# Kernel optimization log

Measured on AMD Instinct MI355X. Metric: run time of the kernel, lower is better.

## Reference

```python
import jax, jax.numpy as jnp
import numpy as np

B, H, S, D = 2, 16, 2048, 64
DEGREE = 2
EPS = 1e-4


def setup_inputs() -> dict:
    key = jax.random.key(0)
    kq, kk, kv = jax.random.split(key, 3)
    q = jax.random.normal(kq, (B, H, S, D), dtype=jnp.float32)
    k = jax.random.normal(kk, (B, H, S, D), dtype=jnp.float32)
    v = jax.random.normal(kv, (B, H, S, D), dtype=jnp.float32)
    return {"q": q, "k": k, "v": v}


def reference(q, k, v):
    # dots: [B,H,S,S] = QK^T
    dots = jnp.einsum("bhsd,bhtd->bhst", q, k)
    # polynomial kernel: x^degree, row-normalized with clamped denom
    x = dots ** DEGREE
    denom = jnp.maximum(x.sum(axis=-1, keepdims=True), EPS)
    attn = x / denom
    # weighted V sum: [B,H,S,D]
    return jnp.einsum("bhst,bhtd->bhsd", attn, v)
```

## Files before the change

kernel.cpp:

```cpp
#include <hip/hip_runtime.h>


#define S_LEN 2048
#define DH    64
#define BQ    128
#define BK    64
#define LSTR  72
#define PSTR  65
#define BH_N  32
#define PER_BH (S_LEN * DH)
#define NT    (S_LEN / BK)

typedef __bf16 bf16x8 __attribute__((ext_vector_type(8)));
typedef __bf16 bf16x2 __attribute__((ext_vector_type(2)));
typedef float  f32x4  __attribute__((ext_vector_type(4)));

__device__ __forceinline__ unsigned short f2bf(float f) {
    union { float f; unsigned int u; } x; x.f = f;
    unsigned int u = x.u;
    return (unsigned short)((u + 0x7fffu + ((u >> 16) & 1u)) >> 16);
}

__device__ __forceinline__ unsigned int pack2bf(float lo, float hi) {
#if __has_builtin(__builtin_amdgcn_cvt_pk_bf16_f32)
    bf16x2 p = __builtin_amdgcn_cvt_pk_bf16_f32(lo, hi);
    union { bf16x2 v; unsigned int u; } c; c.v = p;
    return c.u;
#else
    return (unsigned int)f2bf(lo) | ((unsigned int)f2bf(hi) << 16);
#endif
}

__global__ __launch_bounds__(256)
void prepass_kernel(const float* __restrict__ kg, const float* __restrict__ vg,
                    unsigned short* __restrict__ kbf, unsigned short* __restrict__ vt)
{
    __shared__ unsigned short Ls[64 * PSTR];
    const int tid = threadIdx.x;
    const int bh  = blockIdx.y;
    const int t0  = blockIdx.x * 64;
    const size_t base = (size_t)bh * PER_BH + (size_t)t0 * DH;

    {
        const float4* src = (const float4*)(kg + base + (size_t)tid * 16);
        float4 a = src[0], b = src[1], c = src[2], d = src[3];
        union { unsigned short h[8]; uint4 v; } u0, u1;
        u0.h[0]=f2bf(a.x); u0.h[1]=f2bf(a.y); u0.h[2]=f2bf(a.z); u0.h[3]=f2bf(a.w);
        u0.h[4]=f2bf(b.x); u0.h[5]=f2bf(b.y); u0.h[6]=f2bf(b.z); u0.h[7]=f2bf(b.w);
        u1.h[0]=f2bf(c.x); u1.h[1]=f2bf(c.y); u1.h[2]=f2bf(c.z); u1.h[3]=f2bf(c.w);
        u1.h[4]=f2bf(d.x); u1.h[5]=f2bf(d.y); u1.h[6]=f2bf(d.z); u1.h[7]=f2bf(d.w);
        uint4* dst = (uint4*)(kbf + base + (size_t)tid * 16);
        dst[0] = u0.v; dst[1] = u1.v;
    }

    const float* vb = vg + base;
    #pragma unroll
    for (int r = 0; r < 4; ++r) {
        int idx = r * 256 + tid;
        int row = idx >> 4, c4 = idx & 15;
        float4 f = ((const float4*)vb)[idx];
        unsigned short* p = &Ls[row * PSTR + c4 * 4];
        p[0] = f2bf(f.x); p[1] = f2bf(f.y); p[2] = f2bf(f.z); p[3] = f2bf(f.w);
    }
    __syncthreads();
    #pragma unroll
    for (int r = 0; r < 2; ++r) {
        int idx = r * 256 + tid;
        int d = idx >> 3, j8 = idx & 7;
        union { unsigned short h[8]; uint4 v; } u;
        #pragma unroll
        for (int jj = 0; jj < 8; ++jj) u.h[jj] = Ls[(j8 * 8 + jj) * PSTR + d];
        *(uint4*)(vt + (size_t)bh * PER_BH + (size_t)d * S_LEN + t0 + j8 * 8) = u.v;
    }
}

__global__ __launch_bounds__(256, 2)
void poly_attn_main(const float* __restrict__ qg,
                    const unsigned short* __restrict__ kbf,
                    const unsigned short* __restrict__ vtbf,
                    float* __restrict__ og)
{
    __shared__ unsigned short Ks[2][BK * LSTR];
    __shared__ unsigned short Vts[2][DH * LSTR];
    __shared__ unsigned short Xs[BQ * LSTR];

    const int tid  = threadIdx.x;
    const int lane = tid & 63;
    const int w    = tid >> 6;
    const int c    = lane & 15;
    const int quad = lane >> 4;

    const int bh = blockIdx.y;
    const int q0 = blockIdx.x * BQ;

    const float* qb = qg + ((size_t)bh * S_LEN + q0) * DH;
    const unsigned short* kb  = kbf  + (size_t)bh * PER_BH;
    const unsigned short* vtb = vtbf + (size_t)bh * PER_BH;
    float* ob = og + ((size_t)bh * S_LEN + q0) * DH;

    bf16x8 qfrag[2][2];
    #pragma unroll
    for (int s = 0; s < 2; ++s) {
        #pragma unroll
        for (int kh = 0; kh < 2; ++kh) {
            const float* qp = qb + (32 * w + 16 * s + c) * DH + kh * 32 + quad * 8;
            float4 f0 = *(const float4*)qp;
            float4 f1 = *(const float4*)(qp + 4);
            union { unsigned int d[4]; bf16x8 v; } u;
            u.d[0] = pack2bf(f0.x, f0.y);
            u.d[1] = pack2bf(f0.z, f0.w);
            u.d[2] = pack2bf(f1.x, f1.y);
            u.d[3] = pack2bf(f1.z, f1.w);
            qfrag[s][kh] = u.v;
        }
    }

    f32x4 oacc[2][4];
    #pragma unroll
    for (int s = 0; s < 2; ++s)
        #pragma unroll
        for (int t = 0; t < 4; ++t) {
            oacc[s][t][0]=0.f; oacc[s][t][1]=0.f; oacc[s][t][2]=0.f; oacc[s][t][3]=0.f;
        }
    float dsum[2] = {0.f, 0.f};

    const int srow = tid >> 3;
    const int sc8  = tid & 7;

    uint4 kreg[2], vreg[2];
    #pragma unroll
    for (int it = 0; it < 2; ++it) {
        int row = srow + it * 32;
        kreg[it] = *(const uint4*)(kb + (size_t)row * DH + sc8 * 8);
        vreg[it] = *(const uint4*)(vtb + (size_t)row * S_LEN + sc8 * 8);
    }
    #pragma unroll
    for (int it = 0; it < 2; ++it) {
        int row = srow + it * 32;
        *(uint4*)&Ks[0][row * LSTR + sc8 * 8] = kreg[it];
        *(uint4*)&Vts[0][row * LSTR + sc8 * 8] = vreg[it];
    }
    __syncthreads();

    for (int t = 0; t < NT; ++t) {
        const int cur = t & 1;
        if (t + 1 < NT) {
            const int t0n = (t + 1) * BK;
            #pragma unroll
            for (int it = 0; it < 2; ++it) {
                int row = srow + it * 32;
                kreg[it] = *(const uint4*)(kb + (size_t)(t0n + row) * DH + sc8 * 8);
                vreg[it] = *(const uint4*)(vtb + (size_t)row * S_LEN + t0n + sc8 * 8);
            }
        }

        f32x4 xaccT[2][4];
        #pragma unroll
        for (int s = 0; s < 2; ++s)
            #pragma unroll
            for (int jt = 0; jt < 4; ++jt) {
                xaccT[s][jt][0]=0.f; xaccT[s][jt][1]=0.f; xaccT[s][jt][2]=0.f; xaccT[s][jt][3]=0.f;
            }
        #pragma unroll
        for (int kh = 0; kh < 2; ++kh) {
            #pragma unroll
            for (int jt = 0; jt < 4; ++jt) {
                bf16x8 kfrag = *(const bf16x8*)&Ks[cur][(jt * 16 + c) * LSTR + kh * 32 + quad * 8];
                #pragma unroll
                for (int s = 0; s < 2; ++s)
                    xaccT[s][jt] = __builtin_amdgcn_mfma_f32_16x16x32_bf16(kfrag, qfrag[s][kh], xaccT[s][jt], 0, 0, 0);
            }
        }

        #pragma unroll
        for (int s = 0; s < 2; ++s) {
            #pragma unroll
            for (int jt = 0; jt < 4; ++jt) {
                float x0 = xaccT[s][jt][0], x1 = xaccT[s][jt][1];
                float x2 = xaccT[s][jt][2], x3 = xaccT[s][jt][3];
                x0 *= x0; x1 *= x1; x2 *= x2; x3 *= x3;
                dsum[s] += (x0 + x1) + (x2 + x3);
                uint2 p;
                p.x = pack2bf(x0, x1);
                p.y = pack2bf(x2, x3);
                *(uint2*)&Xs[(32 * w + 16 * s + c) * LSTR + jt * 16 + quad * 4] = p;
            }
        }

        #pragma unroll
        for (int kh = 0; kh < 2; ++kh) {
            bf16x8 aX[2];
            #pragma unroll
            for (int s = 0; s < 2; ++s)
                aX[s] = *(const bf16x8*)&Xs[(32 * w + 16 * s + c) * LSTR + kh * 32 + quad * 8];
            #pragma unroll
            for (int tn = 0; tn < 4; ++tn) {
                bf16x8 vfrag = *(const bf16x8*)&Vts[cur][(tn * 16 + c) * LSTR + kh * 32 + quad * 8];
                #pragma unroll
                for (int s = 0; s < 2; ++s)
                    oacc[s][tn] = __builtin_amdgcn_mfma_f32_16x16x32_bf16(aX[s], vfrag, oacc[s][tn], 0, 0, 0);
            }
        }

        if (t + 1 < NT) {
            #pragma unroll
            for (int it = 0; it < 2; ++it) {
                int row = srow + it * 32;
                *(uint4*)&Ks[cur ^ 1][row * LSTR + sc8 * 8] = kreg[it];
                *(uint4*)&Vts[cur ^ 1][row * LSTR + sc8 * 8] = vreg[it];
            }
            __syncthreads();
        }
    }

    #pragma unroll
    for (int s = 0; s < 2; ++s) {
        float tsum = dsum[s];
        tsum += __shfl_xor(tsum, 16);
        tsum += __shfl_xor(tsum, 32);
        dsum[s] = 1.0f / fmaxf(tsum, 1e-4f);
    }

    #pragma unroll
    for (int s = 0; s < 2; ++s) {
        float inv[4];
        #pragma unroll
        for (int r = 0; r < 4; ++r)
            inv[r] = __shfl(dsum[s], quad * 4 + r);
        #pragma unroll
        for (int tn = 0; tn < 4; ++tn)
            #pragma unroll
            for (int r = 0; r < 4; ++r)
                ob[(32 * w + 16 * s + quad * 4 + r) * DH + tn * 16 + c] = oacc[s][tn][r] * inv[r];
    }
}

__global__ __launch_bounds__(256, 2)
void poly_attn_fallback(const float* __restrict__ qg, const float* __restrict__ kg,
                        const float* __restrict__ vg, float* __restrict__ og)
{
    __shared__ unsigned short Qs[64 * LSTR];
    __shared__ unsigned short Ksl[64 * LSTR];
    __shared__ unsigned short Vt[64 * LSTR];
    __shared__ unsigned short Xsl[64 * LSTR];

    const int tid  = threadIdx.x;
    const int lane = tid & 63;
    const int w    = tid >> 6;
    const int c    = lane & 15;
    const int quad = lane >> 4;
    const int i0   = w * 16;

    const int bh = blockIdx.y;
    const int q0 = blockIdx.x * 64;

    const float* qb = qg + ((size_t)bh * S_LEN + q0) * DH;
    const float* kb = kg + (size_t)bh * S_LEN * DH;
    const float* vb = vg + (size_t)bh * S_LEN * DH;
    float*       ob = og + ((size_t)bh * S_LEN + q0) * DH;

    {
        const float4* qf4 = (const float4*)qb;
        #pragma unroll
        for (int r = 0; r < 4; ++r) {
            int idx = r * 256 + tid;
            int row = idx >> 4, c4 = idx & 15;
            float4 f = qf4[idx];
            ushort4 h;
            h.x = f2bf(f.x); h.y = f2bf(f.y); h.z = f2bf(f.z); h.w = f2bf(f.w);
            *(ushort4*)&Qs[row * LSTR + c4 * 4] = h;
        }
    }

    f32x4 oacc[4];
    #pragma unroll
    for (int t = 0; t < 4; ++t) { oacc[t][0]=0.f; oacc[t][1]=0.f; oacc[t][2]=0.f; oacc[t][3]=0.f; }
    float dsum[4] = {0.f, 0.f, 0.f, 0.f};

    for (int t0 = 0; t0 < S_LEN; t0 += 64) {
        __syncthreads();
        {
            const float4* kf4 = (const float4*)(kb + (size_t)t0 * DH);
            const float4* vf4 = (const float4*)(vb + (size_t)t0 * DH);
            #pragma unroll
            for (int r = 0; r < 4; ++r) {
                int idx = r * 256 + tid;
                int row = idx >> 4, c4 = idx & 15;
                float4 f = kf4[idx];
                ushort4 h;
                h.x = f2bf(f.x); h.y = f2bf(f.y); h.z = f2bf(f.z); h.w = f2bf(f.w);
                *(ushort4*)&Ksl[row * LSTR + c4 * 4] = h;
                float4 g = vf4[idx];
                int d0 = c4 * 4;
                Vt[(d0 + 0) * LSTR + row] = f2bf(g.x);
                Vt[(d0 + 1) * LSTR + row] = f2bf(g.y);
                Vt[(d0 + 2) * LSTR + row] = f2bf(g.z);
                Vt[(d0 + 3) * LSTR + row] = f2bf(g.w);
            }
        }
        __syncthreads();

        f32x4 xacc[4];
        #pragma unroll
        for (int t = 0; t < 4; ++t) { xacc[t][0]=0.f; xacc[t][1]=0.f; xacc[t][2]=0.f; xacc[t][3]=0.f; }
        #pragma unroll
        for (int k0 = 0; k0 < 64; k0 += 32) {
            bf16x8 af = *(const bf16x8*)&Qs[(i0 + c) * LSTR + k0 + quad * 8];
            #pragma unroll
            for (int tn = 0; tn < 4; ++tn) {
                bf16x8 bfg = *(const bf16x8*)&Ksl[(tn * 16 + c) * LSTR + k0 + quad * 8];
                xacc[tn] = __builtin_amdgcn_mfma_f32_16x16x32_bf16(af, bfg, xacc[tn], 0, 0, 0);
            }
        }
        #pragma unroll
        for (int tn = 0; tn < 4; ++tn)
            #pragma unroll
            for (int r = 0; r < 4; ++r) {
                float xv = xacc[tn][r];
                float xs = xv * xv;
                dsum[r] += xs;
                Xsl[(i0 + quad * 4 + r) * LSTR + tn * 16 + c] = f2bf(xs);
            }
        __syncthreads();

        #pragma unroll
        for (int k0 = 0; k0 < 64; k0 += 32) {
            bf16x8 af = *(const bf16x8*)&Xsl[(i0 + c) * LSTR + k0 + quad * 8];
            #pragma unroll
            for (int tn = 0; tn < 4; ++tn) {
                bf16x8 bfg = *(const bf16x8*)&Vt[(tn * 16 + c) * LSTR + k0 + quad * 8];
                oacc[tn] = __builtin_amdgcn_mfma_f32_16x16x32_bf16(af, bfg, oacc[tn], 0, 0, 0);
            }
        }
    }

    #pragma unroll
    for (int r = 0; r < 4; ++r) {
        float s = dsum[r];
        s += __shfl_xor(s, 1);
        s += __shfl_xor(s, 2);
        s += __shfl_xor(s, 4);
        s += __shfl_xor(s, 8);
        dsum[r] = 1.0f / fmaxf(s, 1e-4f);
    }
    #pragma unroll
    for (int tn = 0; tn < 4; ++tn)
        #pragma unroll
        for (int r = 0; r < 4; ++r)
            ob[(i0 + quad * 4 + r) * DH + tn * 16 + c] = oacc[tn][r] * dsum[r];
}

extern "C" void kernel_launch(void* const* d_in, const int* in_sizes, int n_in,
                              void* d_out, int out_size, void* d_ws, size_t ws_size,
                              hipStream_t stream) {
    (void)in_sizes; (void)n_in; (void)out_size;
    const float* q = (const float*)d_in[0];
    const float* k = (const float*)d_in[1];
    const float* v = (const float*)d_in[2];
    float* o = (float*)d_out;

    const size_t elems = (size_t)BH_N * PER_BH;
    const size_t need  = 2 * elems * sizeof(unsigned short);

    if (ws_size >= need) {
        unsigned short* kbf = (unsigned short*)d_ws;
        unsigned short* vtb = kbf + elems;
        prepass_kernel<<<dim3(S_LEN / 64, BH_N), 256, 0, stream>>>(k, v, kbf, vtb);
        poly_attn_main<<<dim3(S_LEN / BQ, BH_N), 256, 0, stream>>>(q, kbf, vtb, o);
    } else {
        poly_attn_fallback<<<dim3(S_LEN / 64, BH_N), 256, 0, stream>>>(q, k, v, o);
    }
}
```

Baseline: 144.2 us.

## Switch main attention loop to 32x32x16 MFMA with register-resident X via permlane32 swap

Rewrites the main kernel to use 32x32x16 bf16 MFMA tiles instead of 16x16x32. The squared scores now feed the second GEMM straight from registers, rearranged with v_permlane32_swap, which removes the Xs shared-memory round trip and its LDS traffic. The output is staged through shared memory so global stores are coalesced float4 writes. The costs are a larger accumulator footprint (f32x16), which may raise register pressure at two blocks per CU, plus an extra barrier in the epilogue.

Result: slower. 159.2 us (+10.4%).

```diff
diff --git a/kernel.cpp b/kernel.cpp
--- a/kernel.cpp
+++ b/kernel.cpp
@@ -6,6 +6,7 @@
 #define BQ    128
 #define BK    64
 #define LSTR  72
+#define EPSTR 68
 #define PSTR  65
 #define BH_N  32
 #define PER_BH (S_LEN * DH)
@@ -14,6 +15,8 @@
 typedef __bf16 bf16x8 __attribute__((ext_vector_type(8)));
 typedef __bf16 bf16x2 __attribute__((ext_vector_type(2)));
 typedef float  f32x4  __attribute__((ext_vector_type(4)));
+typedef float  f32x16 __attribute__((ext_vector_type(16)));
+typedef unsigned int uivec2 __attribute__((ext_vector_type(2)));
 
 __device__ __forceinline__ unsigned short f2bf(float f) {
     union { float f; unsigned int u; } x; x.f = f;
@@ -28,6 +31,15 @@
     return c.u;
 #else
     return (unsigned int)f2bf(lo) | ((unsigned int)f2bf(hi) << 16);
+#endif
+}
+
+__device__ __forceinline__ void pl32swap(unsigned int& a, unsigned int& b) {
+#if __has_builtin(__builtin_amdgcn_permlane32_swap)
+    uivec2 r = __builtin_amdgcn_permlane32_swap(a, b, false, false);
+    a = r[0]; b = r[1];
+#else
+    asm("v_permlane32_swap_b32 %0, %1" : "+v"(a), "+v"(b));
 #endif
 }
 
@@ -80,15 +92,15 @@
                     const unsigned short* __restrict__ vtbf,
                     float* __restrict__ og)
 {
-    __shared__ unsigned short Ks[2][BK * LSTR];
-    __shared__ unsigned short Vts[2][DH * LSTR];
-    __shared__ unsigned short Xs[BQ * LSTR];
+    __shared__ __align__(16) unsigned short smem[4 * 64 * LSTR];
+    #define KS_BASE(b)  ((b) * 64 * LSTR)
+    #define VTS_BASE(b) ((2 + (b)) * 64 * LSTR)
 
     const int tid  = threadIdx.x;
     const int lane = tid & 63;
     const int w    = tid >> 6;
-    const int c    = lane & 15;
-    const int quad = lane >> 4;
+    const int l31  = lane & 31;
+    const int h    = lane >> 5;
 
     const int bh = blockIdx.y;
     const int q0 = blockIdx.x * BQ;
@@ -98,31 +110,26 @@
     const unsigned short* vtb = vtbf + (size_t)bh * PER_BH;
     float* ob = og + ((size_t)bh * S_LEN + q0) * DH;
 
-    bf16x8 qfrag[2][2];
-    #pragma unroll
-    for (int s = 0; s < 2; ++s) {
-        #pragma unroll
-        for (int kh = 0; kh < 2; ++kh) {
-            const float* qp = qb + (32 * w + 16 * s + c) * DH + kh * 32 + quad * 8;
-            float4 f0 = *(const float4*)qp;
-            float4 f1 = *(const float4*)(qp + 4);
-            union { unsigned int d[4]; bf16x8 v; } u;
-            u.d[0] = pack2bf(f0.x, f0.y);
-            u.d[1] = pack2bf(f0.z, f0.w);
-            u.d[2] = pack2bf(f1.x, f1.y);
-            u.d[3] = pack2bf(f1.z, f1.w);
-            qfrag[s][kh] = u.v;
-        }
-    }
-
-    f32x4 oacc[2][4];
-    #pragma unroll
-    for (int s = 0; s < 2; ++s)
-        #pragma unroll
-        for (int t = 0; t < 4; ++t) {
-            oacc[s][t][0]=0.f; oacc[s][t][1]=0.f; oacc[s][t][2]=0.f; oacc[s][t][3]=0.f;
-        }
-    float dsum[2] = {0.f, 0.f};
+    bf16x8 qfrag[4];
+    #pragma unroll
+    for (int ks = 0; ks < 4; ++ks) {
+        const float* qp = qb + (32 * w + l31) * DH + ks * 16 + h * 8;
+        float4 f0 = *(const float4*)qp;
+        float4 f1 = *(const float4*)(qp + 4);
+        union { unsigned int d[4]; bf16x8 v; } u;
+        u.d[0] = pack2bf(f0.x, f0.y);
+        u.d[1] = pack2bf(f0.z, f0.w);
+        u.d[2] = pack2bf(f1.x, f1.y);
+        u.d[3] = pack2bf(f1.z, f1.w);
+        qfrag[ks] = u.v;
+    }
+
+    f32x16 oacc[2];
+    #pragma unroll
+    for (int mt = 0; mt < 2; ++mt)
+        #pragma unroll
+        for (int r = 0; r < 16; ++r) oacc[mt][r] = 0.f;
+    float dsum = 0.f;
 
     const int srow = tid >> 3;
     const int sc8  = tid & 7;
@@ -137,8 +144,8 @@
     #pragma unroll
     for (int it = 0; it < 2; ++it) {
         int row = srow + it * 32;
-        *(uint4*)&Ks[0][row * LSTR + sc8 * 8] = kreg[it];
-        *(uint4*)&Vts[0][row * LSTR + sc8 * 8] = vreg[it];
+        *(uint4*)&smem[KS_BASE(0)  + row * LSTR + sc8 * 8] = kreg[it];
+        *(uint4*)&smem[VTS_BASE(0) + row * LSTR + sc8 * 8] = vreg[it];
     }
     __syncthreads();
 
@@ -154,51 +161,47 @@
             }
         }
 
-        f32x4 xaccT[2][4];
-        #pragma unroll
-        for (int s = 0; s < 2; ++s)
-            #pragma unroll
-            for (int jt = 0; jt < 4; ++jt) {
-                xaccT[s][jt][0]=0.f; xaccT[s][jt][1]=0.f; xaccT[s][jt][2]=0.f; xaccT[s][jt][3]=0.f;
-            }
-        #pragma unroll
-        for (int kh = 0; kh < 2; ++kh) {
-            #pragma unroll
-            for (int jt = 0; jt < 4; ++jt) {
-                bf16x8 kfrag = *(const bf16x8*)&Ks[cur][(jt * 16 + c) * LSTR + kh * 32 + quad * 8];
-                #pragma unroll
-                for (int s = 0; s < 2; ++s)
-                    xaccT[s][jt] = __builtin_amdgcn_mfma_f32_16x16x32_bf16(kfrag, qfrag[s][kh], xaccT[s][jt], 0, 0, 0);
-            }
-        }
-
-        #pragma unroll
-        for (int s = 0; s < 2; ++s) {
-            #pragma unroll
-            for (int jt = 0; jt < 4; ++jt) {
-                float x0 = xaccT[s][jt][0], x1 = xaccT[s][jt][1];
-                float x2 = xaccT[s][jt][2], x3 = xaccT[s][jt][3];
+        unsigned int bfrag[4][4];
+        #pragma unroll
+        for (int jt = 0; jt < 2; ++jt) {
+            f32x16 acc;
+            #pragma unroll
+            for (int r = 0; r < 16; ++r) acc[r] = 0.f;
+            #pragma unroll
+            for (int ks = 0; ks < 4; ++ks) {
+                bf16x8 kf = *(const bf16x8*)&smem[KS_BASE(cur) + (jt * 32 + l31) * LSTR + ks * 16 + h * 8];
+                acc = __builtin_amdgcn_mfma_f32_32x32x16_bf16(kf, qfrag[ks], acc, 0, 0, 0);
+            }
+            unsigned int pk[4][2];
+            #pragma unroll
+            for (int g = 0; g < 4; ++g) {
+                float x0 = acc[4*g+0], x1 = acc[4*g+1], x2 = acc[4*g+2], x3 = acc[4*g+3];
                 x0 *= x0; x1 *= x1; x2 *= x2; x3 *= x3;
-                dsum[s] += (x0 + x1) + (x2 + x3);
-                uint2 p;
-                p.x = pack2bf(x0, x1);
-                p.y = pack2bf(x2, x3);
-                *(uint2*)&Xs[(32 * w + 16 * s + c) * LSTR + jt * 16 + quad * 4] = p;
-            }
-        }
-
-        #pragma unroll
-        for (int kh = 0; kh < 2; ++kh) {
-            bf16x8 aX[2];
-            #pragma unroll
-            for (int s = 0; s < 2; ++s)
-                aX[s] = *(const bf16x8*)&Xs[(32 * w + 16 * s + c) * LSTR + kh * 32 + quad * 8];
-            #pragma unroll
-            for (int tn = 0; tn < 4; ++tn) {
-                bf16x8 vfrag = *(const bf16x8*)&Vts[cur][(tn * 16 + c) * LSTR + kh * 32 + quad * 8];
-                #pragma unroll
-                for (int s = 0; s < 2; ++s)
-                    oacc[s][tn] = __builtin_amdgcn_mfma_f32_16x16x32_bf16(aX[s], vfrag, oacc[s][tn], 0, 0, 0);
+                dsum += (x0 + x1) + (x2 + x3);
+                pk[g][0] = pack2bf(x0, x1);
+                pk[g][1] = pack2bf(x2, x3);
+            }
+            #pragma unroll
+            for (int e = 0; e < 2; ++e) {
+                unsigned int a0 = pk[2*e][0], b0 = pk[2*e+1][0];
+                unsigned int a1 = pk[2*e][1], b1 = pk[2*e+1][1];
+                pl32swap(a0, b0);
+                pl32swap(a1, b1);
+                const int ks = jt * 2 + e;
+                bfrag[ks][0] = a0; bfrag[ks][1] = a1;
+                bfrag[ks][2] = b0; bfrag[ks][3] = b1;
+            }
+        }
+
+        #pragma unroll
+        for (int mt = 0; mt < 2; ++mt) {
+            #pragma unroll
+            for (int ks = 0; ks < 4; ++ks) {
+                bf16x8 vf = *(const bf16x8*)&smem[VTS_BASE(cur) + (mt * 32 + l31) * LSTR + ks * 16 + h * 8];
+                union { unsigned int d[4]; bf16x8 v; } u;
+                u.d[0] = bfrag[ks][0]; u.d[1] = bfrag[ks][1];
+                u.d[2] = bfrag[ks][2]; u.d[3] = bfrag[ks][3];
+                oacc[mt] = __builtin_amdgcn_mfma_f32_32x32x16_bf16(vf, u.v, oacc[mt], 0, 0, 0);
             }
         }
 
@@ -206,33 +209,40 @@
             #pragma unroll
             for (int it = 0; it < 2; ++it) {
                 int row = srow + it * 32;
-                *(uint4*)&Ks[cur ^ 1][row * LSTR + sc8 * 8] = kreg[it];
-                *(uint4*)&Vts[cur ^ 1][row * LSTR + sc8 * 8] = vreg[it];
+                *(uint4*)&smem[KS_BASE(cur ^ 1)  + row * LSTR + sc8 * 8] = kreg[it];
+                *(uint4*)&smem[VTS_BASE(cur ^ 1) + row * LSTR + sc8 * 8] = vreg[it];
             }
             __syncthreads();
         }
     }
 
-    #pragma unroll
-    for (int s = 0; s < 2; ++s) {
-        float tsum = dsum[s];
-        tsum += __shfl_xor(tsum, 16);
-        tsum += __shfl_xor(tsum, 32);
-        dsum[s] = 1.0f / fmaxf(tsum, 1e-4f);
-    }
-
-    #pragma unroll
-    for (int s = 0; s < 2; ++s) {
-        float inv[4];
-        #pragma unroll
-        for (int r = 0; r < 4; ++r)
-            inv[r] = __shfl(dsum[s], quad * 4 + r);
-        #pragma unroll
-        for (int tn = 0; tn < 4; ++tn)
-            #pragma unroll
-            for (int r = 0; r < 4; ++r)
-                ob[(32 * w + 16 * s + quad * 4 + r) * DH + tn * 16 + c] = oacc[s][tn][r] * inv[r];
-    }
+    float tot = dsum + __shfl_xor(dsum, 32);
+    float inv = 1.0f / fmaxf(tot, 1e-4f);
+
+    __syncthreads();
+    float* ep = (float*)smem + (size_t)w * (32 * EPSTR);
+    #pragma unroll
+    for (int mt = 0; mt < 2; ++mt) {
+        #pragma unroll
+        for (int g = 0; g < 4; ++g) {
+            f32x4 vv;
+            vv[0] = oacc[mt][4*g+0] * inv;
+            vv[1] = oacc[mt][4*g+1] * inv;
+            vv[2] = oacc[mt][4*g+2] * inv;
+            vv[3] = oacc[mt][4*g+3] * inv;
+            *(f32x4*)&ep[l31 * EPSTR + mt * 32 + 8 * g + 4 * h] = vv;
+        }
+    }
+    const int quad4 = lane >> 4;
+    const int c4    = lane & 15;
+    #pragma unroll
+    for (int rr = 0; rr < 8; ++rr) {
+        int row = rr * 4 + quad4;
+        f32x4 vv = *(const f32x4*)&ep[row * EPSTR + c4 * 4];
+        *(f32x4*)&ob[(32 * w + row) * DH + c4 * 4] = vv;
+    }
+    #undef KS_BASE
+    #undef VTS_BASE
 }
 
 __global__ __launch_bounds__(256, 2)
@@ -266,9 +276,9 @@
             int idx = r * 256 + tid;
             int row = idx >> 4, c4 = idx & 15;
             float4 f = qf4[idx];
-            ushort4 h;
-            h.x = f2bf(f.x); h.y = f2bf(f.y); h.z = f2bf(f.z); h.w = f2bf(f.w);
-            *(ushort4*)&Qs[row * LSTR + c4 * 4] = h;
+            ushort4 hh;
+            hh.x = f2bf(f.x); hh.y = f2bf(f.y); hh.z = f2bf(f.z); hh.w = f2bf(f.w);
+            *(ushort4*)&Qs[row * LSTR + c4 * 4] = hh;
         }
     }
 
@@ -287,9 +297,9 @@
                 int idx = r * 256 + tid;
                 int row = idx >> 4, c4 = idx & 15;
                 float4 f = kf4[idx];
-                ushort4 h;
-                h.x = f2bf(f.x); h.y = f2bf(f.y); h.z = f2bf(f.z); h.w = f2bf(f.w);
-                *(ushort4*)&Ksl[row * LSTR + c4 * 4] = h;
+                ushort4 hh;
+                hh.x = f2bf(f.x); hh.y = f2bf(f.y); hh.z = f2bf(f.z); hh.w = f2bf(f.w);
+                *(ushort4*)&Ksl[row * LSTR + c4 * 4] = hh;
                 float4 g = vf4[idx];
                 int d0 = c4 * 4;
                 Vt[(d0 + 0) * LSTR + row] = f2bf(g.x);
```
